# Kernel tuning notes

Hardware: AMD Instinct MI355X
Metric: run time of the kernel (lower is better)

## Reference

```python
import jax, jax.numpy as jnp
import numpy as np

N_NODES = 40000
N_EDGES = 640000
FEAT_IN = 128
EDGE_FEAT_IN = 16
HID = 128
N_LAYERS = 4
NUM_GRAPHS = 256


def _linear_params(key, fan_in, fan_out):
    k1, k2 = jax.random.split(key)
    s = 1.0 / np.sqrt(fan_in)
    W = jax.random.uniform(k1, (fan_in, fan_out), jnp.float32, -s, s)
    b = jax.random.uniform(k2, (fan_out,), jnp.float32, -s, s)
    return W, b


def setup_inputs() -> dict:
    key = jax.random.key(0)
    ks = jax.random.split(key, 8)
    h = jax.random.normal(ks[0], (N_NODES, FEAT_IN), jnp.float32)
    e = jax.random.normal(ks[1], (N_EDGES, EDGE_FEAT_IN), jnp.float32)
    edge_index = jax.random.randint(ks[2], (2, N_EDGES), 0, N_NODES, jnp.int32)
    batch = jnp.sort(jax.random.randint(ks[3], (N_NODES,), 0, NUM_GRAPHS, jnp.int32))

    W_embed, b_embed = _linear_params(ks[4], FEAT_IN, HID)
    W_eembed, b_eembed = _linear_params(ks[5], EDGE_FEAT_IN, HID)

    layer_keys = jax.random.split(ks[6], N_LAYERS * 3)
    Wm_l, bm_l, Wh_l, bh_l, We_l, be_l = [], [], [], [], [], []
    for i in range(N_LAYERS):
        Wm, bm = _linear_params(layer_keys[3 * i + 0], 3 * HID, HID)
        Wh, bh = _linear_params(layer_keys[3 * i + 1], 2 * HID, HID)
        We, be = _linear_params(layer_keys[3 * i + 2], 3 * HID, HID)
        Wm_l.append(Wm); bm_l.append(bm)
        Wh_l.append(Wh); bh_l.append(bh)
        We_l.append(We); be_l.append(be)

    return {
        "h": h, "e": e, "edge_index": edge_index, "batch": batch,
        "W_embed": W_embed, "b_embed": b_embed,
        "W_eembed": W_eembed, "b_eembed": b_eembed,
        "Wm": jnp.stack(Wm_l), "bm": jnp.stack(bm_l),
        "Wh": jnp.stack(Wh_l), "bh": jnp.stack(bh_l),
        "We": jnp.stack(We_l), "be": jnp.stack(be_l),
    }


def reference(h, e, W_embed, b_embed, W_eembed, b_eembed,
              Wm, bm, Wh, bh, We, be, edge_index, batch):
    send, rec = edge_index[0], edge_index[1]
    h = h @ W_embed + b_embed          # [N, H]
    e = e @ W_eembed + b_eembed        # [E, H]

    def layer(carry, params):
        h, e = carry
        Wm_i, bm_i, Wh_i, bh_i, We_i, be_i = params
        h_send = h[send]               # [E, H] gather
        h_rec = h[rec]                 # [E, H] gather
        cat3 = jnp.concatenate([h_send, h_rec, e], axis=1)  # [E, 3H]
        messages = cat3 @ Wm_i + bm_i                        # [E, H]
        agg = jax.ops.segment_sum(messages, rec, num_segments=N_NODES)  # scatter_add
        h_new = jnp.concatenate([h, agg], axis=1) @ Wh_i + bh_i
        # NOTE: e_update uses h_send/h_rec from the OLD h, as in the source.
        e_new = cat3 @ We_i + be_i
        return (h_new, e_new), None

    (h, e), _ = jax.lax.scan(layer, (h, e), (Wm, bm, Wh, bh, We, be))
    return jax.ops.segment_sum(h, batch, num_segments=NUM_GRAPHS)  # global_add_pool
```

## Files before the change

### kernel.cpp

```cpp
#include <hip/hip_runtime.h>
#include <hip/hip_bf16.h>

#define NN 40000
#define NE 640000
#define NG 256
#define EW 48

typedef __attribute__((ext_vector_type(8))) short bf16x8;
typedef __attribute__((ext_vector_type(4))) float f32x4;

__device__ __forceinline__ unsigned f2b_u(float f){
  unsigned u = __builtin_bit_cast(unsigned, f);
  u += 0x7fffu + ((u >> 16) & 1u);
  return u >> 16;
}
__device__ __forceinline__ float b2f(unsigned short h){
  unsigned u = ((unsigned)h) << 16;
  return __builtin_bit_cast(float, u);
}
__device__ __forceinline__ unsigned scale_pk(unsigned u, float dg){
  float lo = __builtin_bit_cast(float, u << 16);
  float hi = __builtin_bit_cast(float, u & 0xffff0000u);
  return f2b_u(lo * dg) | (f2b_u(hi * dg) << 16);
}

#define LSTRIDE 147456

__global__ __launch_bounds__(256) void pack2_k(
    const float* __restrict__ Wembed, const float* __restrict__ Wh,
    const float* __restrict__ We, unsigned short* __restrict__ wt,
    unsigned short* __restrict__ wp)
{
  __shared__ float T[64][65];
  const int bx = blockIdx.x;
  const int tx = threadIdx.x & 63, ty = threadIdx.x >> 6;
  const float* src; unsigned short* dst; int rowbase, stride, koff, jt, kt;
  if (bx < 4){
    src = Wembed; dst = wt; rowbase = 0; stride = 128; koff = 0;
    kt = bx & 1; jt = bx >> 1;
  } else {
    const int q = bx - 4, l = q / 24, w = q % 24;
    unsigned short* base = wt + 16384 + (size_t)l * LSTRIDE;
    const float* wh = Wh + (size_t)l * 256 * 128;
    const float* we = We + (size_t)l * 384 * 128;
    if (w < 4){       src = wh; rowbase = 0;   dst = base;          stride = 640; koff = 0;   kt = w & 1;        jt = w >> 1; }
    else if (w < 12){ const int u = w - 4;  src = we; rowbase = 128; dst = base + 81920;  stride = 256; koff = 0;   kt = u & 3; jt = u >> 2; }
    else if (w < 16){ const int u = w - 12; src = we; rowbase = 0;   dst = base + 114688; stride = 256; koff = 0;   kt = u & 1; jt = u >> 1; }
    else if (w < 20){ const int u = w - 16; src = we; rowbase = 256; dst = base + 114688; stride = 256; koff = 128; kt = u & 1; jt = u >> 1; }
    else {            const int u = w - 20; src = wh; rowbase = 128; dst = wp + l * 16384; stride = 128; koff = 0; kt = u & 1; jt = u >> 1; }
  }
  const int k0 = kt * 64, j0 = jt * 64;
  #pragma unroll
  for (int rr = 0; rr < 16; ++rr){
    const int r = ty + rr * 4;
    T[r][tx] = src[(size_t)(rowbase + k0 + r) * 128 + j0 + tx];
  }
  __syncthreads();
  #pragma unroll
  for (int rr = 0; rr < 16; ++rr){
    const int j = ty + rr * 4;
    dst[(size_t)(j0 + j) * stride + koff + k0 + tx] = (unsigned short)f2b_u(T[tx][j]);
  }
}

__global__ __launch_bounds__(256, 2) void prodg_k(
    const float* __restrict__ Wm, const unsigned short* __restrict__ wp,
    unsigned short* __restrict__ wt)
{
  __shared__ unsigned short As[128 * 128];
  __shared__ unsigned short Bs[128 * 128];
  const int l = blockIdx.x / 3, pi = blockIdx.x % 3;
  const int rowoff = (pi == 0) ? 128 : (pi == 1) ? 0 : 256;
  const int poff   = (pi == 0) ? 128 : (pi == 1) ? 256 : 384;
  const float* Am = Wm + (size_t)l * 384 * 128 + (size_t)rowoff * 128;
  const unsigned short* Bt = wp + l * 16384;
  unsigned short* base = wt + 16384 + (size_t)l * LSTRIDE;

  const int tid = threadIdx.x;
  const int lane = tid & 63, wave = tid >> 6;
  const int qm = (wave & 1) << 6, qn = (wave >> 1) << 6;
  const int lr = lane & 15, lkc = lane >> 4;
  const int chunk = tid & 15, r0 = tid >> 4;
  f32x4 acc[4][4] = {};

  #pragma unroll
  for (int rr = 0; rr < 8; ++rr){
    const int r = r0 + rr * 16;
    const float* Af = Am + ((size_t)r << 7) + chunk * 8;
    const float4 f0 = *(const float4*)Af;
    const float4 f1 = *(const float4*)(Af + 4);
    uint4 va;
    va.x = f2b_u(f0.x) | (f2b_u(f0.y) << 16);
    va.y = f2b_u(f0.z) | (f2b_u(f0.w) << 16);
    va.z = f2b_u(f1.x) | (f2b_u(f1.y) << 16);
    va.w = f2b_u(f1.z) | (f2b_u(f1.w) << 16);
    *(uint4*)&As[r * 128 + ((chunk ^ (r & 7)) << 3)] = va;
    *(uint4*)&Bs[r * 128 + ((chunk ^ (r & 7)) << 3)] =
        *(const uint4*)(Bt + (size_t)r * 128 + chunk * 8);
  }
  __syncthreads();
  #pragma unroll
  for (int kk = 0; kk < 4; ++kk){
    const int kc = kk * 4 + lkc;
    bf16x8 af[4], bfr[4];
    #pragma unroll
    for (int mi = 0; mi < 4; ++mi){
      const int r = qm + mi * 16 + lr;
      af[mi] = *(const bf16x8*)&As[r * 128 + ((kc ^ (r & 7)) << 3)];
    }
    #pragma unroll
    for (int ni = 0; ni < 4; ++ni){
      const int r = qn + ni * 16 + lr;
      bfr[ni] = *(const bf16x8*)&Bs[r * 128 + ((kc ^ (r & 7)) << 3)];
    }
    #pragma unroll
    for (int mi = 0; mi < 4; ++mi)
      #pragma unroll
      for (int ni = 0; ni < 4; ++ni)
        acc[mi][ni] = __builtin_amdgcn_mfma_f32_16x16x32_bf16(af[mi], bfr[ni], acc[mi][ni], 0, 0, 0);
  }

  const int rbase = (lane >> 4) << 2;
  #pragma unroll
  for (int mi = 0; mi < 4; ++mi){
    #pragma unroll
    for (int r = 0; r < 4; ++r){
      const int gr = qm + mi * 16 + rbase + r;
      #pragma unroll
      for (int ni = 0; ni < 4; ++ni){
        const int col = qn + ni * 16 + lr;
        const unsigned short b = (unsigned short)f2b_u(acc[mi][ni][r]);
        base[(size_t)col * 640 + poff + gr] = b;
        if (pi == 2) base[(size_t)col * 640 + 512 + gr] = b;
      }
    }
  }
}

__device__ __forceinline__ float dot_b16(const float* __restrict__ cs,
                                         const unsigned short* __restrict__ row){
  float s = 0.f;
  const uint4* r4 = (const uint4*)row;
  #pragma unroll
  for (int q = 0; q < 16; ++q){
    const uint4 v = r4[q];
    s += cs[8*q+0]*b2f((unsigned short)(v.x & 0xffffu)) + cs[8*q+1]*b2f((unsigned short)(v.x >> 16))
       + cs[8*q+2]*b2f((unsigned short)(v.y & 0xffffu)) + cs[8*q+3]*b2f((unsigned short)(v.y >> 16))
       + cs[8*q+4]*b2f((unsigned short)(v.z & 0xffffu)) + cs[8*q+5]*b2f((unsigned short)(v.z >> 16))
       + cs[8*q+6]*b2f((unsigned short)(v.w & 0xffffu)) + cs[8*q+7]*b2f((unsigned short)(v.w >> 16));
  }
  return s;
}

__global__ void vec2_k(const float* __restrict__ bm, const float* __restrict__ be,
                       const unsigned short* __restrict__ wt,
                       const unsigned short* __restrict__ wp, float* __restrict__ rw)
{
  __shared__ float c[128];
  __shared__ float cb[128];
  const int j = threadIdx.x;
  c[j] = 0.f;
  __syncthreads();
  for (int l = 0; l < 4; ++l){
    const unsigned short* base = wt + 16384 + (size_t)l * LSTRIDE;
    cb[j] = bm[l * 128 + j];
    __syncthreads();
    float rwj = dot_b16(cb, wp + l * 16384 + j * 128)
              + dot_b16(c, base + (size_t)j * 640 + 384);
    const float cnj = be[l * 128 + j]
              + dot_b16(c, base + 114688 + (size_t)j * 256 + 128);
    rw[l * 128 + j] = rwj;
    __syncthreads();
    c[j] = cnj;
    __syncthreads();
  }
}

struct YCfg {
  const void* A[5];
  const unsigned short* Bt;
  unsigned short* out0;
  const float* bias;
  const float* rv;
  int np;
  int bstride;
  int scale_mask;
};
struct GArgs { YCfg y[3]; };

template<int AT0>
__global__ __launch_bounds__(256, 2) void gemm_multi(
    GArgs ga, int M, const float* __restrict__ degf)
{
  __shared__ unsigned short As[128 * 128];
  __shared__ unsigned short Bs[128 * 128];
  const YCfg c = ga.y[blockIdx.y];
  const int tid = threadIdx.x;
  const int m0 = blockIdx.x * 128;
  const int lane = tid & 63, wave = tid >> 6;
  const int qm = (wave & 1) << 6, qn = (wave >> 1) << 6;
  const int lr = lane & 15, lkc = lane >> 4;
  const int chunk = tid & 15, r0 = tid >> 4;
  f32x4 acc[4][4] = {};

  for (int p = 0; p < c.np; ++p){
    if (p) __syncthreads();
    const unsigned short* Ab = (const unsigned short*)c.A[p];
    const bool scl = (c.scale_mask >> p) & 1;
    #pragma unroll
    for (int rr = 0; rr < 8; ++rr){
      const int r = r0 + rr * 16;
      const int gr = m0 + r;
      uint4 va = make_uint4(0u, 0u, 0u, 0u);
      if (gr < M){
        if (AT0 && p == 0){
          const float* Af = (const float*)c.A[0] + ((size_t)gr << 7) + chunk * 8;
          const float4 f0 = *(const float4*)Af;
          const float4 f1 = *(const float4*)(Af + 4);
          va.x = f2b_u(f0.x) | (f2b_u(f0.y) << 16);
          va.y = f2b_u(f0.z) | (f2b_u(f0.w) << 16);
          va.z = f2b_u(f1.x) | (f2b_u(f1.y) << 16);
          va.w = f2b_u(f1.z) | (f2b_u(f1.w) << 16);
        } else {
          va = *(const uint4*)(Ab + ((size_t)gr << 7) + chunk * 8);
          if (scl){
            const float dg = degf[gr];
            va.x = scale_pk(va.x, dg); va.y = scale_pk(va.y, dg);
            va.z = scale_pk(va.z, dg); va.w = scale_pk(va.w, dg);
          }
        }
      }
      *(uint4*)&As[r * 128 + ((chunk ^ (r & 7)) << 3)] = va;
      *(uint4*)&Bs[r * 128 + ((chunk ^ (r & 7)) << 3)] =
          *(const uint4*)(c.Bt + (size_t)r * c.bstride + p * 128 + chunk * 8);
    }
    __syncthreads();
    #pragma unroll
    for (int kk = 0; kk < 4; ++kk){
      const int kc = kk * 4 + lkc;
      bf16x8 af[4], bfr[4];
      #pragma unroll
      for (int mi = 0; mi < 4; ++mi){
        const int r = qm + mi * 16 + lr;
        af[mi] = *(const bf16x8*)&As[r * 128 + ((kc ^ (r & 7)) << 3)];
      }
      #pragma unroll
      for (int ni = 0; ni < 4; ++ni){
        const int r = qn + ni * 16 + lr;
        bfr[ni] = *(const bf16x8*)&Bs[r * 128 + ((kc ^ (r & 7)) << 3)];
      }
      #pragma unroll
      for (int mi = 0; mi < 4; ++mi)
        #pragma unroll
        for (int ni = 0; ni < 4; ++ni)
          acc[mi][ni] = __builtin_amdgcn_mfma_f32_16x16x32_bf16(af[mi], bfr[ni], acc[mi][ni], 0, 0, 0);
    }
  }

  const int rbase = (lane >> 4) << 2;
  #pragma unroll
  for (int mi = 0; mi < 4; ++mi){
    #pragma unroll
    for (int r = 0; r < 4; ++r){
      const int gr = m0 + qm + mi * 16 + rbase + r;
      if (gr >= M) continue;
      const size_t ro = (size_t)gr << 7;
      float dg = 0.f;
      if (c.rv) dg = degf[gr];
      #pragma unroll
      for (int ni = 0; ni < 4; ++ni){
        const int col = qn + ni * 16 + lr;
        float v = acc[mi][ni][r];
        if (c.bias) v += c.bias[col];
        if (c.rv)   v += dg * c.rv[col];
        c.out0[ro + col] = (unsigned short)f2b_u(v);
      }
    }
  }
}

__global__ void fill_ell_k(const int* __restrict__ rec, const int* __restrict__ send,
                           int* __restrict__ cnt, int* __restrict__ ell_s,
                           int* __restrict__ ell_e){
  const int i = blockIdx.x * 256 + threadIdx.x;
  if (i < NE){
    const int r = rec[i];
    const int k = atomicAdd(&cnt[r], 1);
    if (k < EW){
      ell_s[r * EW + k] = send[i];
      ell_e[r * EW + k] = i;
    }
  }
}

__global__ void aux_k(const int* __restrict__ cnt, float* __restrict__ degf,
                      const int* __restrict__ batch, int* __restrict__ gptr){
  const int b = blockIdx.x, t = threadIdx.x;
  if (b < 157){
    const int i = b * 256 + t;
    if (i < NN) degf[i] = (float)cnt[i];
  } else {
    if (t < NG){
      int lo = 0, hi = NN;
      while (lo < hi){
        const int mid = (lo + hi) >> 1;
        if (batch[mid] < t) lo = mid + 1; else hi = mid;
      }
      gptr[t] = lo;
      if (t == 0) gptr[NG] = NN;
    }
  }
}

__global__ void sraw_ell_k(const int* __restrict__ cnt, const int* __restrict__ ell_e,
                           const float* __restrict__ e_in, float* __restrict__ sraw)
{
  const int n = blockIdx.x * 16 + (threadIdx.x >> 4);
  const int c16 = threadIdx.x & 15;
  const int m = cnt[n];
  const int* row = ell_e + n * EW;
  float acc = 0.f;
  int j = 0;
  for (; j + 2 <= m; j += 2){
    const int e0 = row[j], e1 = row[j + 1];
    acc += e_in[(size_t)e0 * 16 + c16] + e_in[(size_t)e1 * 16 + c16];
  }
  if (j < m) acc += e_in[(size_t)row[j] * 16 + c16];
  sraw[(size_t)n * 16 + c16] = acc;
}

__global__ void s0_k(const float* __restrict__ sraw, const float* __restrict__ W,
                     const float* __restrict__ b, const int* __restrict__ cnt,
                     unsigned short* __restrict__ TPS)
{
  __shared__ float Ws[2048];
  __shared__ float bs[128];
  const int t = threadIdx.x;
  for (int i = t; i < 2048; i += 256) Ws[i] = W[i];
  if (t < 128) bs[t] = b[t];
  __syncthreads();
  const int half = t >> 7, j = t & 127;
  const int n = blockIdx.x * 2 + half;
  const float* sr = sraw + (size_t)n * 16;
  const float dg = (float)cnt[n];
  float acc = dg * bs[j];
  #pragma unroll
  for (int k = 0; k < 16; ++k) acc += sr[k] * Ws[k * 128 + j];
  TPS[((size_t)n << 7) + j] = (unsigned short)f2b_u(acc);
}

__global__ __launch_bounds__(256) void gather_k(
    const int* __restrict__ cnt, const int* __restrict__ ell_s,
    const unsigned short* __restrict__ hb, unsigned short* __restrict__ tb)
{
  const int n = blockIdx.x * 4 + (threadIdx.x >> 6);
  const int lane = threadIdx.x & 63;
  const int half = lane >> 5, l32 = lane & 31;
  const int m = cnt[n];
  const unsigned short* colp = hb + 4 * l32;
  const int myidx = (lane < m) ? ell_s[n * EW + lane] : 0;
  float a0 = 0.f, a1 = 0.f, a2 = 0.f, a3 = 0.f;
  int k = 0;
  for (; k + 16 <= m; k += 16){
    int s[8];
    #pragma unroll
    for (int u = 0; u < 8; ++u) s[u] = __shfl(myidx, k + 2 * u + half);
    uint2 v[8];
    #pragma unroll
    for (int u = 0; u < 8; ++u) v[u] = *(const uint2*)(colp + ((size_t)s[u] << 7));
    #pragma unroll
    for (int u = 0; u < 8; ++u){
      a0 += b2f((unsigned short)(v[u].x & 0xffffu));
      a1 += b2f((unsigned short)(v[u].x >> 16));
      a2 += b2f((unsigned short)(v[u].y & 0xffffu));
      a3 += b2f((unsigned short)(v[u].y >> 16));
    }
  }
  for (; k + 4 <= m; k += 4){
    const int s0 = __shfl(myidx, k + half);
    const int s1 = __shfl(myidx, k + 2 + half);
    const uint2 v0 = *(const uint2*)(colp + ((size_t)s0 << 7));
    const uint2 v1 = *(const uint2*)(colp + ((size_t)s1 << 7));
    a0 += b2f((unsigned short)(v0.x & 0xffffu)) + b2f((unsigned short)(v1.x & 0xffffu));
    a1 += b2f((unsigned short)(v0.x >> 16)) + b2f((unsigned short)(v1.x >> 16));
    a2 += b2f((unsigned short)(v0.y & 0xffffu)) + b2f((unsigned short)(v1.y & 0xffffu));
    a3 += b2f((unsigned short)(v0.y >> 16)) + b2f((unsigned short)(v1.y >> 16));
  }
  for (; k < m; k += 2){
    if (k + half < m){
      const int s = __shfl(myidx, k + half);
      const uint2 v = *(const uint2*)(colp + ((size_t)s << 7));
      a0 += b2f((unsigned short)(v.x & 0xffffu));
      a1 += b2f((unsigned short)(v.x >> 16));
      a2 += b2f((unsigned short)(v.y & 0xffffu));
      a3 += b2f((unsigned short)(v.y >> 16));
    }
  }
  a0 += __shfl_xor(a0, 32); a1 += __shfl_xor(a1, 32);
  a2 += __shfl_xor(a2, 32); a3 += __shfl_xor(a3, 32);
  if (half == 0){
    uint2 o;
    o.x = f2b_u(a0) | (f2b_u(a1) << 16);
    o.y = f2b_u(a2) | (f2b_u(a3) << 16);
    *(uint2*)(tb + ((size_t)n << 7) + 4 * l32) = o;
  }
}

__global__ void pool_k(const int* __restrict__ gptr, const unsigned short* __restrict__ hb,
                       float* __restrict__ out)
{
  const int g = blockIdx.x * 4 + (threadIdx.x >> 6);
  const int lane = threadIdx.x & 63;
  float a0 = 0.f, a1 = 0.f;
  for (int n = gptr[g]; n < gptr[g + 1]; ++n){
    const unsigned v = *(const unsigned*)(hb + ((size_t)n << 7) + 2 * lane);
    a0 += b2f((unsigned short)(v & 0xffffu));
    a1 += b2f((unsigned short)(v >> 16));
  }
  float2 r; r.x = a0; r.y = a1;
  *(float2*)(out + (size_t)g * 128 + 2 * lane) = r;
}

extern "C" void kernel_launch(void* const* d_in, const int* in_sizes, int n_in,
                              void* d_out, int out_size, void* d_ws, size_t ws_size,
                              hipStream_t stream)
{
  const float* h_in     = (const float*)d_in[0];
  const float* e_in     = (const float*)d_in[1];
  const int*   eidx     = (const int*)d_in[2];
  const int*   batch    = (const int*)d_in[3];
  const float* W_embed  = (const float*)d_in[4];
  const float* b_embed  = (const float*)d_in[5];
  const float* W_eembed = (const float*)d_in[6];
  const float* b_eembed = (const float*)d_in[7];
  const float* Wm       = (const float*)d_in[8];
  const float* bm       = (const float*)d_in[9];
  const float* Wh       = (const float*)d_in[10];
  const float* bh       = (const float*)d_in[11];
  const float* We       = (const float*)d_in[12];
  const float* be       = (const float*)d_in[13];
  const int* send = eidx;
  const int* rec  = eidx + NE;

  char* ws = (char*)d_ws;
  size_t off = 0;
  auto alloc = [&](size_t bytes) -> char* {
    char* p = ws + off;
    off = (off + bytes + 255) & ~(size_t)255;
    return p;
  };
  unsigned short* wt  = (unsigned short*)alloc((size_t)(16384 + 4 * LSTRIDE) * 2);
  unsigned short* wp  = (unsigned short*)alloc((size_t)4 * 16384 * 2);
  unsigned short* hA  = (unsigned short*)alloc((size_t)NN * 128 * 2);
  unsigned short* hB  = (unsigned short*)alloc((size_t)NN * 128 * 2);
  unsigned short* Q0  = (unsigned short*)alloc((size_t)NN * 128 * 2);
  unsigned short* Q1  = (unsigned short*)alloc((size_t)NN * 128 * 2);
  unsigned short* T0  = (unsigned short*)alloc((size_t)NN * 128 * 2);
  unsigned short* T1  = (unsigned short*)alloc((size_t)NN * 128 * 2);
  unsigned short* tb  = (unsigned short*)alloc((size_t)NN * 128 * 2);
  float* rw   = (float*)alloc((size_t)512 * 4);
  int* cnt    = (int*)alloc((size_t)NN * 4);
  float* degf = (float*)alloc((size_t)NN * 4);
  int* gptr   = (int*)alloc((size_t)(NG + 1) * 4);
  int* ell_s  = (int*)alloc((size_t)NN * EW * 4);
  int*   ell_e = (int*)tb;
  float* sraw  = (float*)hB;

  if (off > ws_size) return;

  const dim3 B256(256);

  pack2_k<<<dim3(100), B256, 0, stream>>>(W_embed, Wh, We, wt, wp);
  prodg_k<<<dim3(12), B256, 0, stream>>>(Wm, wp, wt);
  vec2_k<<<dim3(1), dim3(128), 0, stream>>>(bm, be, wt, wp, rw);

  hipMemsetAsync(cnt, 0, (size_t)NN * 4, stream);
  fill_ell_k<<<dim3(2500), B256, 0, stream>>>(rec, send, cnt, ell_s, ell_e);
  aux_k<<<dim3(158), B256, 0, stream>>>(cnt, degf, batch, gptr);
  sraw_ell_k<<<dim3(NN / 16), B256, 0, stream>>>(cnt, ell_e, e_in, sraw);
  s0_k<<<dim3(NN / 2), B256, 0, stream>>>(sraw, W_eembed, b_eembed, cnt, T0);

  {
    GArgs ga = {};
    ga.y[0].A[0] = h_in; ga.y[0].Bt = wt; ga.y[0].out0 = hA;
    ga.y[0].bias = b_embed; ga.y[0].np = 1; ga.y[0].bstride = 128;
    ga.y[0].scale_mask = 0;
    gemm_multi<1><<<dim3(313, 1), B256, 0, stream>>>(ga, NN, degf);
  }

  unsigned short* hc = hA;  unsigned short* hn = hB;
  unsigned short* Qc = Q0;  unsigned short* Qn = Q1;
  unsigned short* Tc = T0;  unsigned short* Tn = T1;
  for (int l = 0; l < 4; ++l){
    const unsigned short* LB = wt + 16384 + (size_t)l * LSTRIDE;

    gather_k<<<dim3(NN / 4), B256, 0, stream>>>(cnt, ell_s, hc, tb);

    GArgs ga = {};
    YCfg& y0 = ga.y[0];
    y0.A[0] = hc; y0.A[1] = hc; y0.A[2] = tb; y0.A[3] = Tc; y0.A[4] = Qc;
    y0.Bt = LB; y0.out0 = hn; y0.bias = bh + l * 128; y0.rv = rw + l * 128;
    y0.np = (l == 0) ? 4 : 5;
    y0.bstride = 640; y0.scale_mask = (1 << 1) | (1 << 4);
    int ny = 1;
    if (l < 3){
      YCfg& y1 = ga.y[1];
      y1.A[0] = hc; y1.A[1] = Qc; y1.Bt = LB + 81920;
      y1.out0 = Qn; y1.np = (l == 0) ? 1 : 2; y1.bstride = 256; y1.scale_mask = 0;
      YCfg& y2 = ga.y[2];
      y2.A[0] = tb; y2.A[1] = Tc; y2.Bt = LB + 114688;
      y2.out0 = Tn; y2.np = 2; y2.bstride = 256; y2.scale_mask = 0;
      ny = 3;
    }
    gemm_multi<0><<<dim3(313, ny), B256, 0, stream>>>(ga, NN, degf);

    unsigned short* t2;
    t2 = hc; hc = hn; hn = t2;
    t2 = Qc; Qc = Qn; Qn = t2;
    t2 = Tc; Tc = Tn; Tn = t2;
  }

  pool_k<<<dim3(NG / 4), B256, 0, stream>>>(gptr, hc, (float*)d_out);
}
```

Baseline: 676.9 us.

## Parallelize weight-vector precompute, fuse edge-sum kernels, interleave ELL, split gather into passes

Replaces the single-block 128-thread bias-propagation kernel with a 1024-thread version that stages the weight rows in shared memory and reduces partial dot products. Packs sender and edge indices into one int2 ELL array, and fuses the raw edge-feature sum with the edge-embedding projection so the intermediate buffer is no longer written and reread. Splits the neighbour gather into four column-slice passes via a 2D grid, each lane loading 4 bytes for more parallelism per node. This spends more gather blocks and repeated index loads in exchange for shorter serial chains, and clamps neighbour counts to the ELL width.

```diff
diff --git a/kernel.cpp b/kernel.cpp
--- a/kernel.cpp
+++ b/kernel.cpp
@@ -137,41 +137,53 @@
   }
 }
 
-__device__ __forceinline__ float dot_b16(const float* __restrict__ cs,
-                                         const unsigned short* __restrict__ row){
-  float s = 0.f;
-  const uint4* r4 = (const uint4*)row;
-  #pragma unroll
-  for (int q = 0; q < 16; ++q){
-    const uint4 v = r4[q];
-    s += cs[8*q+0]*b2f((unsigned short)(v.x & 0xffffu)) + cs[8*q+1]*b2f((unsigned short)(v.x >> 16))
-       + cs[8*q+2]*b2f((unsigned short)(v.y & 0xffffu)) + cs[8*q+3]*b2f((unsigned short)(v.y >> 16))
-       + cs[8*q+4]*b2f((unsigned short)(v.z & 0xffffu)) + cs[8*q+5]*b2f((unsigned short)(v.z >> 16))
-       + cs[8*q+6]*b2f((unsigned short)(v.w & 0xffffu)) + cs[8*q+7]*b2f((unsigned short)(v.w >> 16));
-  }
-  return s;
-}
-
-__global__ void vec2_k(const float* __restrict__ bm, const float* __restrict__ be,
-                       const unsigned short* __restrict__ wt,
-                       const unsigned short* __restrict__ wp, float* __restrict__ rw)
-{
-  __shared__ float c[128];
-  __shared__ float cb[128];
-  const int j = threadIdx.x;
-  c[j] = 0.f;
-  __syncthreads();
+__global__ __launch_bounds__(1024, 1) void vec2b_k(
+    const float* __restrict__ bm, const float* __restrict__ be,
+    const unsigned short* __restrict__ wt, const unsigned short* __restrict__ wp,
+    float* __restrict__ rw)
+{
+  __shared__ unsigned short s_wp[16384];
+  __shared__ unsigned short s_m3[16384];
+  __shared__ unsigned short s_w3[16384];
+  __shared__ float c[128], cb[128];
+  __shared__ float part_rw[128][8], part_cn[128][8];
+  const int t = threadIdx.x;
+  const int j = t >> 3, p = t & 7;
+  if (t < 128) c[t] = 0.f;
+
   for (int l = 0; l < 4; ++l){
     const unsigned short* base = wt + 16384 + (size_t)l * LSTRIDE;
-    cb[j] = bm[l * 128 + j];
+    ((uint4*)s_wp)[t]        = ((const uint4*)(wp + l * 16384))[t];
+    ((uint4*)s_wp)[t + 1024] = ((const uint4*)(wp + l * 16384))[t + 1024];
+    {
+      const uint4* srcm = (const uint4*)(base + (size_t)j * 640 + 384);
+      ((uint4*)(s_m3 + j * 128))[p * 2]     = srcm[p * 2];
+      ((uint4*)(s_m3 + j * 128))[p * 2 + 1] = srcm[p * 2 + 1];
+      const uint4* srcw = (const uint4*)(base + 114688 + (size_t)j * 256 + 128);
+      ((uint4*)(s_w3 + j * 128))[p * 2]     = srcw[p * 2];
+      ((uint4*)(s_w3 + j * 128))[p * 2 + 1] = srcw[p * 2 + 1];
+    }
+    if (t < 128) cb[t] = bm[l * 128 + t];
     __syncthreads();
-    float rwj = dot_b16(cb, wp + l * 16384 + j * 128)
-              + dot_b16(c, base + (size_t)j * 640 + 384);
-    const float cnj = be[l * 128 + j]
-              + dot_b16(c, base + 114688 + (size_t)j * 256 + 128);
-    rw[l * 128 + j] = rwj;
+    float prw = 0.f, pcn = 0.f;
+    #pragma unroll
+    for (int q = 0; q < 16; ++q){
+      const int kk = p * 16 + q;
+      prw += cb[kk] * b2f(s_wp[j * 128 + kk]) + c[kk] * b2f(s_m3[j * 128 + kk]);
+      pcn += c[kk] * b2f(s_w3[j * 128 + kk]);
+    }
+    part_rw[j][p] = prw; part_cn[j][p] = pcn;
     __syncthreads();
-    c[j] = cnj;
+    if (t < 128){
+      float rwj = 0.f, cnj = be[l * 128 + t];
+      #pragma unroll
+      for (int i = 0; i < 8; ++i){ rwj += part_rw[t][i]; cnj += part_cn[t][i]; }
+      rw[l * 128 + t] = rwj;
+      __syncthreads();
+      c[t] = cnj;
+    } else {
+      __syncthreads();
+    }
     __syncthreads();
   }
 }
@@ -280,16 +292,12 @@
 }
 
 __global__ void fill_ell_k(const int* __restrict__ rec, const int* __restrict__ send,
-                           int* __restrict__ cnt, int* __restrict__ ell_s,
-                           int* __restrict__ ell_e){
+                           int* __restrict__ cnt, int2* __restrict__ ell){
   const int i = blockIdx.x * 256 + threadIdx.x;
   if (i < NE){
     const int r = rec[i];
     const int k = atomicAdd(&cnt[r], 1);
-    if (k < EW){
-      ell_s[r * EW + k] = send[i];
-      ell_e[r * EW + k] = i;
-    }
+    if (k < EW) ell[r * EW + k] = make_int2(send[i], i);
   }
 }
 
@@ -312,98 +320,75 @@
   }
 }
 
-__global__ void sraw_ell_k(const int* __restrict__ cnt, const int* __restrict__ ell_e,
-                           const float* __restrict__ e_in, float* __restrict__ sraw)
-{
-  const int n = blockIdx.x * 16 + (threadIdx.x >> 4);
-  const int c16 = threadIdx.x & 15;
-  const int m = cnt[n];
-  const int* row = ell_e + n * EW;
-  float acc = 0.f;
-  int j = 0;
-  for (; j + 2 <= m; j += 2){
-    const int e0 = row[j], e1 = row[j + 1];
-    acc += e_in[(size_t)e0 * 16 + c16] + e_in[(size_t)e1 * 16 + c16];
-  }
-  if (j < m) acc += e_in[(size_t)row[j] * 16 + c16];
-  sraw[(size_t)n * 16 + c16] = acc;
-}
-
-__global__ void s0_k(const float* __restrict__ sraw, const float* __restrict__ W,
-                     const float* __restrict__ b, const int* __restrict__ cnt,
-                     unsigned short* __restrict__ TPS)
-{
+__global__ __launch_bounds__(256) void sraw_s0_k(
+    const int* __restrict__ cnt, const int2* __restrict__ ell,
+    const float* __restrict__ e_in, const float* __restrict__ W,
+    const float* __restrict__ bias, unsigned short* __restrict__ TPS)
+{
+  __shared__ float sums[16][16];
+  __shared__ float dgs[16];
   __shared__ float Ws[2048];
   __shared__ float bs[128];
   const int t = threadIdx.x;
+  const int n0 = blockIdx.x * 16;
   for (int i = t; i < 2048; i += 256) Ws[i] = W[i];
-  if (t < 128) bs[t] = b[t];
+  if (t < 128) bs[t] = bias[t];
+  {
+    const int a = t >> 4, c16 = t & 15;
+    const int n = n0 + a;
+    const int m0 = cnt[n];
+    const int m = (m0 < EW) ? m0 : EW;
+    const int2* row = ell + n * EW;
+    float acc = 0.f;
+    int j = 0;
+    for (; j + 2 <= m; j += 2){
+      const int e0 = row[j].y, e1 = row[j + 1].y;
+      acc += e_in[(size_t)e0 * 16 + c16] + e_in[(size_t)e1 * 16 + c16];
+    }
+    if (j < m) acc += e_in[(size_t)row[j].y * 16 + c16];
+    sums[a][c16] = acc;
+    if (c16 == 0) dgs[a] = (float)m0;
+  }
   __syncthreads();
-  const int half = t >> 7, j = t & 127;
-  const int n = blockIdx.x * 2 + half;
-  const float* sr = sraw + (size_t)n * 16;
-  const float dg = (float)cnt[n];
-  float acc = dg * bs[j];
-  #pragma unroll
-  for (int k = 0; k < 16; ++k) acc += sr[k] * Ws[k * 128 + j];
-  TPS[((size_t)n << 7) + j] = (unsigned short)f2b_u(acc);
-}
-
-__global__ __launch_bounds__(256) void gather_k(
-    const int* __restrict__ cnt, const int* __restrict__ ell_s,
+  #pragma unroll
+  for (int i = 0; i < 8; ++i){
+    const int o = t + 256 * i;
+    const int node = o >> 7, col = o & 127;
+    float acc = dgs[node] * bs[col];
+    #pragma unroll
+    for (int k = 0; k < 16; ++k) acc += sums[node][k] * Ws[k * 128 + col];
+    TPS[((size_t)(n0 + node) << 7) + col] = (unsigned short)f2b_u(acc);
+  }
+}
+
+__global__ __launch_bounds__(256) void gather_q_k(
+    const int* __restrict__ cnt, const int2* __restrict__ ell,
     const unsigned short* __restrict__ hb, unsigned short* __restrict__ tb)
 {
+  const int pass = blockIdx.y;
   const int n = blockIdx.x * 4 + (threadIdx.x >> 6);
   const int lane = threadIdx.x & 63;
-  const int half = lane >> 5, l32 = lane & 31;
-  const int m = cnt[n];
-  const unsigned short* colp = hb + 4 * l32;
-  const int myidx = (lane < m) ? ell_s[n * EW + lane] : 0;
-  float a0 = 0.f, a1 = 0.f, a2 = 0.f, a3 = 0.f;
-  int k = 0;
-  for (; k + 16 <= m; k += 16){
-    int s[8];
-    #pragma unroll
-    for (int u = 0; u < 8; ++u) s[u] = __shfl(myidx, k + 2 * u + half);
-    uint2 v[8];
-    #pragma unroll
-    for (int u = 0; u < 8; ++u) v[u] = *(const uint2*)(colp + ((size_t)s[u] << 7));
-    #pragma unroll
-    for (int u = 0; u < 8; ++u){
-      a0 += b2f((unsigned short)(v[u].x & 0xffffu));
-      a1 += b2f((unsigned short)(v[u].x >> 16));
-      a2 += b2f((unsigned short)(v[u].y & 0xffffu));
-      a3 += b2f((unsigned short)(v[u].y >> 16));
-    }
-  }
-  for (; k + 4 <= m; k += 4){
-    const int s0 = __shfl(myidx, k + half);
-    const int s1 = __shfl(myidx, k + 2 + half);
-    const uint2 v0 = *(const uint2*)(colp + ((size_t)s0 << 7));
-    const uint2 v1 = *(const uint2*)(colp + ((size_t)s1 << 7));
-    a0 += b2f((unsigned short)(v0.x & 0xffffu)) + b2f((unsigned short)(v1.x & 0xffffu));
-    a1 += b2f((unsigned short)(v0.x >> 16)) + b2f((unsigned short)(v1.x >> 16));
-    a2 += b2f((unsigned short)(v0.y & 0xffffu)) + b2f((unsigned short)(v1.y & 0xffffu));
-    a3 += b2f((unsigned short)(v0.y >> 16)) + b2f((unsigned short)(v1.y >> 16));
-  }
-  for (; k < m; k += 2){
-    if (k + half < m){
-      const int s = __shfl(myidx, k + half);
-      const uint2 v = *(const uint2*)(colp + ((size_t)s << 7));
-      a0 += b2f((unsigned short)(v.x & 0xffffu));
-      a1 += b2f((unsigned short)(v.x >> 16));
-      a2 += b2f((unsigned short)(v.y & 0xffffu));
-      a3 += b2f((unsigned short)(v.y >> 16));
-    }
-  }
-  a0 += __shfl_xor(a0, 32); a1 += __shfl_xor(a1, 32);
-  a2 += __shfl_xor(a2, 32); a3 += __shfl_xor(a3, 32);
-  if (half == 0){
-    uint2 o;
-    o.x = f2b_u(a0) | (f2b_u(a1) << 16);
-    o.y = f2b_u(a2) | (f2b_u(a3) << 16);
-    *(uint2*)(tb + ((size_t)n << 7) + 4 * l32) = o;
-  }
+  const int grp = lane >> 4, l16 = lane & 15;
+  const int mc = cnt[n];
+  const int m = (mc < EW) ? mc : EW;
+  const int idx = (lane < m) ? ell[n * EW + lane].x : 0;
+  const unsigned short* cp = hb + pass * 32 + (l16 << 1);
+  float a0 = 0.f, a1 = 0.f;
+  for (int k = 0; k < m; k += 8){
+    const int kk0 = k + grp, kk1 = k + 4 + grp;
+    const int s0 = __shfl(idx, kk0 < m ? kk0 : 0);
+    const int s1 = __shfl(idx, kk1 < m ? kk1 : 0);
+    unsigned v0 = 0u, v1 = 0u;
+    if (kk0 < m) v0 = *(const unsigned*)(cp + ((size_t)s0 << 7));
+    if (kk1 < m) v1 = *(const unsigned*)(cp + ((size_t)s1 << 7));
+    a0 += b2f((unsigned short)(v0 & 0xffffu)) + b2f((unsigned short)(v1 & 0xffffu));
+    a1 += b2f((unsigned short)(v0 >> 16)) + b2f((unsigned short)(v1 >> 16));
+  }
+  a0 += __shfl_xor(a0, 16); a0 += __shfl_xor(a0, 32);
+  a1 += __shfl_xor(a1, 16); a1 += __shfl_xor(a1, 32);
+  if (grp == 0)
+    *(unsigned*)(tb + ((size_t)n << 7) + pass * 32 + (l16 << 1)) =
+        f2b_u(a0) | (f2b_u(a1) << 16);
 }
 
 __global__ void pool_k(const int* __restrict__ gptr, const unsigned short* __restrict__ hb,
@@ -462,9 +447,7 @@
   int* cnt    = (int*)alloc((size_t)NN * 4);
   float* degf = (float*)alloc((size_t)NN * 4);
   int* gptr   = (int*)alloc((size_t)(NG + 1) * 4);
-  int* ell_s  = (int*)alloc((size_t)NN * EW * 4);
-  int*   ell_e = (int*)tb;
-  float* sraw  = (float*)hB;
+  int2* ell   = (int2*)alloc((size_t)NN * EW * 8);
 
   if (off > ws_size) return;
 
@@ -472,13 +455,12 @@
 
   pack2_k<<<dim3(100), B256, 0, stream>>>(W_embed, Wh, We, wt, wp);
   prodg_k<<<dim3(12), B256, 0, stream>>>(Wm, wp, wt);
-  vec2_k<<<dim3(1), dim3(128), 0, stream>>>(bm, be, wt, wp, rw);
+  vec2b_k<<<dim3(1), dim3(1024), 0, stream>>>(bm, be, wt, wp, rw);
 
   hipMemsetAsync(cnt, 0, (size_t)NN * 4, stream);
-  fill_ell_k<<<dim3(2500), B256, 0, stream>>>(rec, send, cnt, ell_s, ell_e);
+  fill_ell_k<<<dim3(2500), B256, 0, stream>>>(rec, send, cnt, ell);
   aux_k<<<dim3(158), B256, 0, stream>>>(cnt, degf, batch, gptr);
-  sraw_ell_k<<<dim3(NN / 16), B256, 0, stream>>>(cnt, ell_e, e_in, sraw);
-  s0_k<<<dim3(NN / 2), B256, 0, stream>>>(sraw, W_eembed, b_eembed, cnt, T0);
+  sraw_s0_k<<<dim3(NN / 16), B256, 0, stream>>>(cnt, ell, e_in, W_eembed, b_eembed, T0);
 
   {
     GArgs ga = {};
@@ -494,7 +476,7 @@
   for (int l = 0; l < 4; ++l){
     const unsigned short* LB = wt + 16384 + (size_t)l * LSTRIDE;
 
-    gather_k<<<dim3(NN / 4), B256, 0, stream>>>(cnt, ell_s, hc, tb);
+    gather_q_k<<<dim3(NN / 4, 4), B256, 0, stream>>>(cnt, ell, hc, tb);
 
     GArgs ga = {};
     YCfg& y0 = ga.y[0];
```

Measured after the change: 697.2 us. 1.03x slower.
